# Optimization experiments

Measured on AMD Instinct MI355X. Metric: run time of the kernel, lower is better.

## Reference

```python
import jax, jax.numpy as jnp
import numpy as np

D = 2048
N = 16384
E = 8
THRESHOLD = 0.5


def setup_inputs() -> dict:
    key = jax.random.key(0)
    ks = jax.random.split(key, 6)
    x = jax.random.normal(ks[0], (N, D), dtype=jnp.float32)
    # pretrained weight + truncated SVD basis (frozen in original module)
    W_np = np.asarray(jax.random.normal(ks[1], (D, D), dtype=jnp.float32))
    U, S, Vt = np.linalg.svd(W_np, full_matrices=False)
    k = int((np.cumsum(S) < THRESHOLD * S.sum()).sum())  # energy-threshold rank
    U_k = jnp.asarray(U[:, :k])
    V_k = jnp.asarray(Vt.T[:, :k])  # torch.svd returns V, not V^T
    W = jnp.asarray(W_np)
    lambda_k = jax.random.normal(ks[2], (E, k), dtype=jnp.float32)
    v = jnp.zeros((D,), dtype=jnp.float32)
    W_g1 = jax.random.normal(ks[3], (k, 1), dtype=jnp.float32)
    W_g2 = jax.random.normal(ks[4], (1, E), dtype=jnp.float32)
    return {"x": x, "W": W, "U_k": U_k, "V_k": V_k, "lambda_k": lambda_k,
            "v": v, "W_g1": W_g1, "W_g2": W_g2}


def reference(x, W, U_k, V_k, lambda_k, v, W_g1, W_g2):
    # Routing: g = softmax((x @ U_k) @ W_g1 @ W_g2)  -> [N, E]
    xu = x @ U_k                                   # [N, k] (shared with delta path)
    g = jax.nn.softmax((xu @ W_g1) @ W_g2, axis=-1)
    # sum_i g_i * (x @ (W + U diag(lam_i) V^T))
    #   = (x@W) * sum_i g_i  +  ((x@U) * (g @ lam)) @ V^T   (low-rank factored)
    base = x @ W                                   # [N, D], computed once
    coef = g @ lambda_k                            # [N, k]
    out = base * jnp.sum(g, axis=-1, keepdims=True) + (xu * coef) @ V_k.T
    return out * (1.0 + v)
```

## Files before the change

kernel.cpp:

```cpp
#include <hip/hip_runtime.h>
#include <hip/hip_bf16.h>

#define D_DIM 2048
#define E_DIM 8

typedef __attribute__((ext_vector_type(8))) short short8;
typedef __attribute__((ext_vector_type(4))) float f32x4;

__device__ __forceinline__ unsigned short f2bf(float f) {
  union { float f; unsigned int u; } v; v.f = f;
  unsigned int u = v.u;
  u += 0x7FFFu + ((u >> 16) & 1u);
  return (unsigned short)(u >> 16);
}

__device__ __forceinline__ void async_copy16(const void* g, void* l) {
  __builtin_amdgcn_global_load_lds((const __attribute__((address_space(1))) void*)g,
                                   (__attribute__((address_space(3))) void*)l,
                                   16, 0, 0);
}

__global__ void k_cvt_bf16(const float* __restrict__ in,
                           unsigned short* __restrict__ out, long long n) {
  long long i = ((long long)blockIdx.x * blockDim.x + threadIdx.x) * 8;
  const long long stride = (long long)gridDim.x * blockDim.x * 8;
  for (; i < n; i += stride) {
    float4 a = *(const float4*)(in + i);
    float4 b = *(const float4*)(in + i + 4);
    short8 r;
    r[0] = (short)f2bf(a.x); r[1] = (short)f2bf(a.y);
    r[2] = (short)f2bf(a.z); r[3] = (short)f2bf(a.w);
    r[4] = (short)f2bf(b.x); r[5] = (short)f2bf(b.y);
    r[6] = (short)f2bf(b.z); r[7] = (short)f2bf(b.w);
    *(short8*)(out + i) = r;
  }
}

__global__ void k_transpose_bf16(const float* __restrict__ in, int in_rows, int in_cols,
                                 int in_ld, unsigned short* __restrict__ out, int out_rows) {
  __shared__ float tile[32][33];
  const int tx = threadIdx.x;
  const int ty = threadIdx.y;
  const int c = blockIdx.x * 32 + tx;
  #pragma unroll
  for (int i = 0; i < 4; ++i) {
    const int r = blockIdx.y * 32 + ty + i * 8;
    float vv = 0.0f;
    if (r < in_rows && c < in_cols) vv = in[(size_t)r * in_ld + c];
    tile[ty + i * 8][tx] = vv;
  }
  __syncthreads();
  const int oc = blockIdx.y * 32 + tx;
  #pragma unroll
  for (int i = 0; i < 4; ++i) {
    const int orow = blockIdx.x * 32 + ty + i * 8;
    if (orow < out_rows && oc < in_rows)
      out[(size_t)orow * in_rows + oc] = f2bf(tile[tx][ty + i * 8]);
  }
}

__global__ void k_pad_bf16(const float* __restrict__ in, unsigned short* __restrict__ out,
                           int rows, int cols, int cols_pad) {
  long long idx = (long long)blockIdx.x * blockDim.x + threadIdx.x;
  const long long total = (long long)rows * cols_pad;
  const long long stride = (long long)gridDim.x * blockDim.x;
  for (; idx < total; idx += stride) {
    const int r = (int)(idx / cols_pad);
    const int c = (int)(idx % cols_pad);
    out[idx] = (c < cols) ? f2bf(in[(size_t)r * cols + c]) : (unsigned short)0;
  }
}

__global__ void k_route(const float* __restrict__ xu, int k, int k_pad,
                        const float* __restrict__ Wg1, const float* __restrict__ Wg2,
                        const float* __restrict__ lam,
                        unsigned short* __restrict__ A2, float* __restrict__ rowscale,
                        int Nrows) {
  const int w = threadIdx.x >> 6;
  const int lane = threadIdx.x & 63;
  const int row = blockIdx.x * 4 + w;
  if (row >= Nrows) return;
  const float* xr = xu + (size_t)row * k_pad;
  float s = 0.0f;
  for (int kk = lane; kk < k; kk += 64) s += xr[kk] * Wg1[kk];
  #pragma unroll
  for (int off = 32; off; off >>= 1) s += __shfl_xor(s, off);
  float lg[E_DIM];
  float mx = -INFINITY;
  #pragma unroll
  for (int e = 0; e < E_DIM; ++e) { lg[e] = s * Wg2[e]; mx = fmaxf(mx, lg[e]); }
  float Z = 0.0f;
  #pragma unroll
  for (int e = 0; e < E_DIM; ++e) { lg[e] = expf(lg[e] - mx); Z += lg[e]; }
  float g[E_DIM]; float gsum = 0.0f;
  #pragma unroll
  for (int e = 0; e < E_DIM; ++e) { g[e] = lg[e] / Z; gsum += g[e]; }
  const float inv = 1.0f / gsum;
  if (lane == 0) rowscale[row] = gsum;
  unsigned short* arow = A2 + (size_t)row * k_pad;
  for (int kk = lane; kk < k_pad; kk += 64) {
    if (kk < k) {
      float c = 0.0f;
      #pragma unroll
      for (int e = 0; e < E_DIM; ++e) c += g[e] * lam[(size_t)e * k + kk];
      arow[kk] = f2bf(xr[kk] * (c * inv));
    } else {
      arow[kk] = 0;
    }
  }
}

template<int EPI>
__global__ __launch_bounds__(256, 2) void k_gemm(
    const unsigned short* __restrict__ A0, int lda0,
    const unsigned short* __restrict__ A1, int lda1,
    const unsigned short* __restrict__ B0, int ldb0,
    const unsigned short* __restrict__ B1, int ldb1,
    int ka0, int Ktot,
    float* __restrict__ Cout, int ldc,
    const float* __restrict__ rowscale, const float* __restrict__ vcol) {
  __shared__ unsigned short As[128 * 32];
  __shared__ unsigned short Bs[128 * 32];
  const int tid = threadIdx.x;
  const int lane = tid & 63;
  const int w = tid >> 6;
  const int brow = blockIdx.x * 128;
  const int bcol = blockIdx.y * 128;

  f32x4 acc[4][4];
  #pragma unroll
  for (int m = 0; m < 4; ++m)
    #pragma unroll
    for (int n2 = 0; n2 < 4; ++n2)
      #pragma unroll
      for (int j = 0; j < 4; ++j) acc[m][n2][j] = 0.0f;

  const int srow = lane >> 2;
  const int scol = (lane & 3) * 8;
  const int wr = (w >> 1) * 64;
  const int wc = (w & 1) * 64;
  const int nkt = Ktot >> 5;

  for (int kt = 0; kt < nkt; ++kt) {
    const int k0 = kt * 32;
    const unsigned short* Ab; int ldA; int kA;
    const unsigned short* Bb; int ldB; int kB;
    if (k0 < ka0) { Ab = A0; ldA = lda0; kA = k0;       Bb = B0; ldB = ldb0; kB = k0; }
    else          { Ab = A1; ldA = lda1; kA = k0 - ka0; Bb = B1; ldB = ldb1; kB = k0 - ka0; }
    __syncthreads();
    #pragma unroll
    for (int p = 0; p < 2; ++p) {
      const int c = p * 4 + w;
      const int row = c * 16 + srow;
      async_copy16(Ab + (size_t)(brow + row) * ldA + kA + scol, (void*)(As + c * 512));
      async_copy16(Bb + (size_t)(bcol + row) * ldB + kB + scol, (void*)(Bs + c * 512));
    }
    __syncthreads();
    short8 av[4], bv[4];
    #pragma unroll
    for (int m = 0; m < 4; ++m)
      av[m] = *(const short8*)(As + (wr + m * 16 + (lane & 15)) * 32 + (lane >> 4) * 8);
    #pragma unroll
    for (int n2 = 0; n2 < 4; ++n2)
      bv[n2] = *(const short8*)(Bs + (wc + n2 * 16 + (lane & 15)) * 32 + (lane >> 4) * 8);
    #pragma unroll
    for (int m = 0; m < 4; ++m)
      #pragma unroll
      for (int n2 = 0; n2 < 4; ++n2)
        acc[m][n2] = __builtin_amdgcn_mfma_f32_16x16x32_bf16(av[m], bv[n2], acc[m][n2], 0, 0, 0);
  }

  #pragma unroll
  for (int m = 0; m < 4; ++m) {
    #pragma unroll
    for (int n2 = 0; n2 < 4; ++n2) {
      const int col = bcol + wc + n2 * 16 + (lane & 15);
      float cs = 1.0f;
      if (EPI == 1) cs = 1.0f + vcol[col];
      #pragma unroll
      for (int j = 0; j < 4; ++j) {
        const int row = brow + wr + m * 16 + (lane >> 4) * 4 + j;
        float val = acc[m][n2][j];
        if (EPI == 1) val *= rowscale[row] * cs;
        Cout[(size_t)row * ldc + col] = val;
      }
    }
  }
}

extern "C" void kernel_launch(void* const* d_in, const int* in_sizes, int n_in,
                              void* d_out, int out_size, void* d_ws, size_t ws_size,
                              hipStream_t stream) {
  const float* x   = (const float*)d_in[0];
  const float* W   = (const float*)d_in[1];
  const float* U   = (const float*)d_in[2];
  const float* V   = (const float*)d_in[3];
  const float* lam = (const float*)d_in[4];
  const float* v   = (const float*)d_in[5];
  const float* Wg1 = (const float*)d_in[6];
  const float* Wg2 = (const float*)d_in[7];
  float* out = (float*)d_out;

  const int N = in_sizes[0] / D_DIM;
  const int k = in_sizes[2] / D_DIM;
  const int k_pad = (k + 127) & ~127;

  char* ws = (char*)d_ws;
  size_t off = 0;
  auto alloc = [&](size_t bytes) -> void* {
    void* p = ws + off;
    off += (bytes + 255) & ~(size_t)255;
    return p;
  };
  unsigned short* xb  = (unsigned short*)alloc((size_t)N * D_DIM * 2);
  unsigned short* Wt  = (unsigned short*)alloc((size_t)D_DIM * D_DIM * 2);
  unsigned short* Ukt = (unsigned short*)alloc((size_t)k_pad * D_DIM * 2);
  unsigned short* Vb  = (unsigned short*)alloc((size_t)D_DIM * k_pad * 2);
  float*          xu  = (float*)alloc((size_t)N * k_pad * 4);
  unsigned short* A2  = (unsigned short*)alloc((size_t)N * k_pad * 2);
  float*          rs  = (float*)alloc((size_t)N * 4);
  if (off > ws_size) return;

  k_cvt_bf16<<<2048, 256, 0, stream>>>(x, xb, (long long)N * D_DIM);
  k_transpose_bf16<<<dim3(D_DIM / 32, D_DIM / 32), dim3(32, 8), 0, stream>>>(
      W, D_DIM, D_DIM, D_DIM, Wt, D_DIM);
  k_transpose_bf16<<<dim3(k_pad / 32, D_DIM / 32), dim3(32, 8), 0, stream>>>(
      U, D_DIM, k, k, Ukt, k_pad);
  k_pad_bf16<<<512, 256, 0, stream>>>(V, Vb, D_DIM, k, k_pad);

  k_gemm<0><<<dim3(N / 128, k_pad / 128), 256, 0, stream>>>(
      xb, D_DIM, nullptr, 0,
      Ukt, D_DIM, nullptr, 0,
      D_DIM, D_DIM,
      xu, k_pad, nullptr, nullptr);

  k_route<<<N / 4, 256, 0, stream>>>(xu, k, k_pad, Wg1, Wg2, lam, A2, rs, N);

  k_gemm<1><<<dim3(N / 128, D_DIM / 128), 256, 0, stream>>>(
      xb, D_DIM, A2, k_pad,
      Wt, D_DIM, Vb, k_pad,
      D_DIM, D_DIM + k_pad,
      out, D_DIM, rs, v);
}
```

Baseline: 383.6 us.

## Use 256x256-tile 8-wave GEMM with 4-stage async LDS pipeline for main product

Adds a new GEMM kernel with 256x256 output tiles, 512 threads and a 4-buffer global_load_lds pipeline that prefetches three K-steps ahead. The A and B loads are split across two MFMA phases, with swizzled LDS addressing and an XCD-aware block remap. It replaces the 128x128 kernel for the large fused base-plus-low-rank GEMM. The goal is more operand reuse per tile and better overlap of memory with MFMA, at the cost of higher register and LDS pressure.

After: 348.9 us. 9.0% less time.

```diff
diff --git a/kernel.cpp b/kernel.cpp
--- a/kernel.cpp
+++ b/kernel.cpp
@@ -188,6 +188,153 @@
   }
 }
 
+template<int EPI>
+__global__ __launch_bounds__(512, 2) void k_gemm256(
+    const unsigned short* __restrict__ A0, int lda0,
+    const unsigned short* __restrict__ A1, int lda1,
+    const unsigned short* __restrict__ B0, int ldb0,
+    const unsigned short* __restrict__ B1, int ldb1,
+    int ka0, int Ktot, int gridM,
+    float* __restrict__ Cout, int ldc,
+    const float* __restrict__ rowscale, const float* __restrict__ vcol) {
+  __shared__ unsigned short lds[4 * 16384];
+  const int tid = threadIdx.x;
+  const int lane = tid & 63;
+  const int w = tid >> 6;
+  const int wm = w >> 2;
+  const int wn = w & 3;
+
+  int bid = blockIdx.x;
+  const int cpx = gridDim.x >> 3;
+  bid = (bid & 7) * cpx + (bid >> 3);
+  const int bx = bid % gridM;
+  const int by = bid / gridM;
+  const long long brow = (long long)bx * 256;
+  const long long bcol = (long long)by * 256;
+
+  const int c0 = w * 2;
+  const int sr0 = lane >> 2;
+  const int sj  = lane & 3;
+
+  auto stage = [&](int tt, const unsigned short* P, long long ldP, int kbase,
+                   long long rbase, int breg) {
+    unsigned short* dst = lds + (tt & 3) * 16384 + breg * 8192;
+    #pragma unroll
+    for (int c = 0; c < 2; ++c) {
+      const int chunk = c0 + c;
+      const int lrow = chunk * 16 + sr0;
+      const int jj = sj ^ ((lrow >> 1) & 3);
+      const unsigned short* src = P + (rbase + lrow) * ldP + kbase + jj * 8;
+      async_copy16(src, (void*)(dst + chunk * 512));
+    }
+  };
+
+  const int NT = Ktot >> 5;
+
+  auto segA = [&](int tt, const unsigned short*& P, long long& ld, int& kb) {
+    const int k0 = tt * 32;
+    if (k0 < ka0) { P = A0; ld = lda0; kb = k0; }
+    else          { P = A1; ld = lda1; kb = k0 - ka0; }
+  };
+  auto segB = [&](int tt, const unsigned short*& P, long long& ld, int& kb) {
+    const int k0 = tt * 32;
+    if (k0 < ka0) { P = B0; ld = ldb0; kb = k0; }
+    else          { P = B1; ld = ldb1; kb = k0 - ka0; }
+  };
+
+  for (int p = 0; p < 3; ++p) {
+    const unsigned short* PA; long long ldA; int kA; segA(p, PA, ldA, kA);
+    const unsigned short* PB; long long ldB; int kB; segB(p, PB, ldB, kB);
+    stage(p, PA, ldA, kA, brow, 0);
+    stage(p, PB, ldB, kB, bcol, 1);
+  }
+  asm volatile("s_waitcnt vmcnt(8)" ::: "memory");
+  __builtin_amdgcn_s_barrier();
+
+  f32x4 acc[8][4];
+  #pragma unroll
+  for (int m = 0; m < 8; ++m)
+    #pragma unroll
+    for (int n = 0; n < 4; ++n)
+      #pragma unroll
+      for (int j = 0; j < 4; ++j) acc[m][n][j] = 0.0f;
+
+  const int l15 = lane & 15;
+  const int jhi = lane >> 4;
+
+  for (int t = 0; t < NT; ++t) {
+    const unsigned short* Areg = lds + (t & 3) * 16384;
+    const unsigned short* Breg = Areg + 8192;
+    short8 av[8], bv[2];
+
+    #pragma unroll
+    for (int m = 0; m < 8; ++m) {
+      const int row = wm * 128 + m * 16 + l15;
+      const int jj = jhi ^ ((row >> 1) & 3);
+      av[m] = *(const short8*)(Areg + row * 32 + jj * 8);
+    }
+    #pragma unroll
+    for (int n = 0; n < 2; ++n) {
+      const int row = wn * 64 + n * 16 + l15;
+      const int jj = jhi ^ ((row >> 1) & 3);
+      bv[n] = *(const short8*)(Breg + row * 32 + jj * 8);
+    }
+    if (t + 3 < NT) {
+      const unsigned short* PA; long long ldA; int kA; segA(t + 3, PA, ldA, kA);
+      stage(t + 3, PA, ldA, kA, brow, 0);
+    }
+    __builtin_amdgcn_s_barrier();
+    __builtin_amdgcn_s_setprio(1);
+    #pragma unroll
+    for (int m = 0; m < 8; ++m)
+      #pragma unroll
+      for (int n = 0; n < 2; ++n)
+        acc[m][n] = __builtin_amdgcn_mfma_f32_16x16x32_bf16(av[m], bv[n], acc[m][n], 0, 0, 0);
+    __builtin_amdgcn_s_setprio(0);
+    __builtin_amdgcn_s_barrier();
+
+    #pragma unroll
+    for (int n = 0; n < 2; ++n) {
+      const int row = wn * 64 + 32 + n * 16 + l15;
+      const int jj = jhi ^ ((row >> 1) & 3);
+      bv[n] = *(const short8*)(Breg + row * 32 + jj * 8);
+    }
+    if (t + 3 < NT) {
+      const unsigned short* PB; long long ldB; int kB; segB(t + 3, PB, ldB, kB);
+      stage(t + 3, PB, ldB, kB, bcol, 1);
+    }
+    __builtin_amdgcn_s_barrier();
+    __builtin_amdgcn_s_setprio(1);
+    #pragma unroll
+    for (int m = 0; m < 8; ++m)
+      #pragma unroll
+      for (int n = 0; n < 2; ++n)
+        acc[m][2 + n] = __builtin_amdgcn_mfma_f32_16x16x32_bf16(av[m], bv[n], acc[m][2 + n], 0, 0, 0);
+    __builtin_amdgcn_s_setprio(0);
+    if (t + 3 < NT)      asm volatile("s_waitcnt vmcnt(8)" ::: "memory");
+    else if (t + 2 < NT) asm volatile("s_waitcnt vmcnt(4)" ::: "memory");
+    else if (t + 1 < NT) asm volatile("s_waitcnt vmcnt(0)" ::: "memory");
+    __builtin_amdgcn_s_barrier();
+  }
+
+  #pragma unroll
+  for (int m = 0; m < 8; ++m) {
+    #pragma unroll
+    for (int n = 0; n < 4; ++n) {
+      const long long col = bcol + wn * 64 + n * 16 + l15;
+      float cs = 1.0f;
+      if (EPI == 1) cs = 1.0f + vcol[col];
+      #pragma unroll
+      for (int j = 0; j < 4; ++j) {
+        const long long row = brow + wm * 128 + m * 16 + jhi * 4 + j;
+        float val = acc[m][n][j];
+        if (EPI == 1) val *= rowscale[row] * cs;
+        Cout[row * ldc + col] = val;
+      }
+    }
+  }
+}
+
 extern "C" void kernel_launch(void* const* d_in, const int* in_sizes, int n_in,
                               void* d_out, int out_size, void* d_ws, size_t ws_size,
                               hipStream_t stream) {
@@ -236,9 +383,11 @@
 
   k_route<<<N / 4, 256, 0, stream>>>(xu, k, k_pad, Wg1, Wg2, lam, A2, rs, N);
 
-  k_gemm<1><<<dim3(N / 128, D_DIM / 128), 256, 0, stream>>>(
+  const int gridM = N / 256;
+  const int gridN = D_DIM / 256;
+  k_gemm256<1><<<gridM * gridN, 512, 0, stream>>>(
       xb, D_DIM, A2, k_pad,
       Wt, D_DIM, Vb, k_pad,
-      D_DIM, D_DIM + k_pad,
+      D_DIM, D_DIM + k_pad, gridM,
       out, D_DIM, rs, v);
 }
```
